# Performance work log

Measured on AMD Instinct MI355X. Metric: run time of the kernel, lower is better.

## Reference

```python
import jax, jax.numpy as jnp
import numpy as np

GAMMA = 0.99
EPS = 1e-05
B, D, K, C = 65536, 512, 1024, 100


def setup_inputs() -> dict:
    key = jax.random.key(0)
    k1, k2, k3, k4, k5 = jax.random.split(key, 5)
    return {
        "batch_vectors": jax.random.normal(k1, (B, D), dtype=jnp.float32),
        "batch_keys_id": jax.random.randint(k2, (B,), 0, C, dtype=jnp.int32),
        "weight": jax.random.normal(k3, (D, K), dtype=jnp.float32),
        "cluster_size": jnp.ones((K,), dtype=jnp.float32),
        "embed_avg": jax.random.normal(k4, (D, K), dtype=jnp.float32),
        "hist": jax.random.uniform(k5, (K, C), dtype=jnp.float32),
    }


def reference(batch_vectors, batch_keys_id, weight, cluster_size, embed_avg, hist):
    # --- find_nearest_centroids: euclidean distance to each codebook column ---
    x_sq = jnp.sum(batch_vectors * batch_vectors, axis=1, keepdims=True)      # [B,1]
    w_sq = jnp.sum(weight * weight, axis=0, keepdims=True)                    # [1,K]
    d2 = x_sq - 2.0 * (batch_vectors @ weight) + w_sq                         # [B,K]
    dist = jnp.sqrt(jnp.maximum(d2, 0.0))
    argmin = jnp.argmin(dist, axis=-1)                                        # [B]

    # --- one-hot counts and embed_sum (scatter-add form of flatten @ onehot) ---
    n_idx_choice = jax.ops.segment_sum(
        jnp.ones((B,), dtype=batch_vectors.dtype), argmin, num_segments=K)    # [K]
    n_idx_choice = jnp.where(n_idx_choice == 0, 1.0, n_idx_choice)
    embed_sum = jax.ops.segment_sum(batch_vectors, argmin, num_segments=K).T  # [D,K]

    # --- EMA updates ---
    new_cluster_size = cluster_size * GAMMA + (1.0 - GAMMA) * n_idx_choice
    new_embed_avg = embed_avg * GAMMA + (1.0 - GAMMA) * embed_sum
    n = jnp.sum(new_cluster_size)
    cs_norm = (new_cluster_size + EPS) / (n + K * EPS) * n                    # [K]
    new_weight = new_embed_avg / cs_norm[None, :]                             # [D,K]

    # --- update_hist: per-cluster class histogram (scatter-add) ---
    batch_hist = jnp.zeros((K, C), dtype=hist.dtype).at[argmin, batch_keys_id].add(1.0)
    new_hist = hist * GAMMA + (1.0 - GAMMA) * batch_hist

    return new_weight, new_cluster_size, new_embed_avg, new_hist, argmin
```

## Files before the change

### kernel.cpp

```cpp
#include <hip/hip_runtime.h>
#include <hip/hip_fp16.h>


#define NB 65536
#define ND 512
#define NK 1024
#define NC 100
#define TAU 0.25f
#define FLAG_CAP 16384
#define FROWS 8
#define GROWS 128

typedef unsigned int u32;
typedef unsigned short u16;
typedef unsigned long long u64;
typedef __attribute__((ext_vector_type(8))) _Float16 half8v;
typedef __attribute__((ext_vector_type(4))) float f32x4;

#define OFF_COUNTS   0
#define OFF_CURSOR   1024
#define OFF_BHIST    2048
#define OFF_FLAGCNT  104448
#define OFF_WSQ      104512
#define OFF_ZERO_END 105536
#define OFF_FLAGLIST 105536
#define OFF_FKEYS    121920
#define OFF_CSNORM   154688
#define OFF_OFFSETS  155712
#define OFF_ARGMIN   156736
#define OFF_ORDER    222272
#define OFF_KORDER   287808
#define OFF_WTHI     353344
#define OFF_WT32     615488
#define OFF_XH       1139776
#define OFF_ESUM     17916992

__device__ inline f32x4 mfma16f(half8v a, half8v b, f32x4 c) {
  return __builtin_amdgcn_mfma_f32_16x16x32_f16(a, b, c, 0, 0, 0);
}

__device__ __forceinline__ void gl_lds16(const u16* g, u16* l) {
  __builtin_amdgcn_global_load_lds(
      (const __attribute__((address_space(1))) u32*)g,
      (__attribute__((address_space(3))) u32*)l, 16, 0, 0);
}

__device__ inline u32 f32_sortable(float f) {
  u32 b = __float_as_uint(f);
  return (b & 0x80000000u) ? ~b : (b | 0x80000000u);
}

__device__ inline half8v cvt8_f16(const float4& a, const float4& b) {
  half8v h;
  h[0] = (_Float16)a.x; h[1] = (_Float16)a.y;
  h[2] = (_Float16)a.z; h[3] = (_Float16)a.w;
  h[4] = (_Float16)b.x; h[5] = (_Float16)b.y;
  h[6] = (_Float16)b.z; h[7] = (_Float16)b.w;
  return h;
}

__global__ __launch_bounds__(256) void prep_x(const float* __restrict__ X,
                                              u16* __restrict__ Xh) {
  size_t i = ((size_t)blockIdx.x * 256 + threadIdx.x) * 8;
  float4 a = *(const float4*)(X + i);
  float4 b = *(const float4*)(X + i + 4);
  *(half8v*)(Xh + i) = cvt8_f16(a, b);
}

__global__ __launch_bounds__(256) void prep_w(const float* __restrict__ W,
                                              u16* __restrict__ Wthi,
                                              float* __restrict__ Wt32,
                                              float* __restrict__ wsq) {
  __shared__ float tile[32][33];
  int db = blockIdx.x & 15;
  int kb = blockIdx.x >> 4;
  int tx = threadIdx.x & 31, ty = threadIdx.x >> 5;
  float s = 0.f;
#pragma unroll
  for (int i = 0; i < 4; ++i) {
    int d = db * 32 + ty + 8 * i;
    float wv = W[(size_t)d * NK + kb * 32 + tx];
    tile[ty + 8 * i][tx] = wv;
    s += wv * wv;
  }
  atomicAdd(&wsq[kb * 32 + tx], s);
  __syncthreads();
#pragma unroll
  for (int i = 0; i < 4; ++i) {
    int kl = ty + 8 * i;
    float f = tile[tx][kl];
    size_t o = (size_t)(kb * 32 + kl) * ND + db * 32 + tx;
    Wt32[o] = f;
    Wthi[o] = __half_as_ushort(__float2half(f));
  }
}

__global__ __launch_bounds__(256, 2) void argmin_pair(
    const u16* __restrict__ Xh, const u16* __restrict__ Wthi,
    const float* __restrict__ wsq, const int* __restrict__ cls,
    int* __restrict__ argmin_i, float* __restrict__ argmin_f,
    int* __restrict__ counts, float* __restrict__ bhist,
    int* __restrict__ flagCnt, int* __restrict__ flagList) {
  __shared__ __align__(16) u16 Ah[2 * 128 * 64];
  __shared__ __align__(16) u16 Bh[2 * 256 * 32];
  __shared__ float wsq_s[NK];
  __shared__ float redV[128][2];
  __shared__ float redS[128][2];
  __shared__ int redI[128][2];

  const int t = threadIdx.x;
  const int lane = t & 63;
  const int w = t >> 6;
  const int g = lane >> 4;
  const int l15 = lane & 15;
  const int wrb = (w >> 1) * 64;
  const int wcb = (w & 1) * 128;
  const int brow = blockIdx.x * 128;

#pragma unroll
  for (int i = 0; i < 4; ++i) wsq_s[t + 256 * i] = wsq[t + 256 * i];

  const int sub = lane >> 3;
  const int c8p = lane & 7;
  const size_t asrc = (size_t)(brow + w * 32 + sub) * ND + (size_t)((c8p ^ sub) * 8);

  const int rp = lane >> 2;
  const int bcl = (lane & 3) ^ (rp & 3);
  const size_t bsrc = (size_t)(w * 64 + rp) * ND + (size_t)(bcl * 8);

  int aofs[2];
#pragma unroll
  for (int kk = 0; kk < 2; ++kk)
    aofs[kk] = (wrb + l15) * 64 + (((kk * 4 + g) ^ (l15 & 7)) * 8);
  const int bofs = (wcb + l15) * 32 + ((g ^ (l15 & 3)) * 8);

  float bestV[4][4], secV[4][4];
  int bestI[4][4];
#pragma unroll
  for (int m = 0; m < 4; ++m)
#pragma unroll
    for (int r = 0; r < 4; ++r) {
      bestV[m][r] = 3.4e38f; secV[m][r] = 3.4e38f; bestI[m][r] = 0;
    }

  f32x4 acc[4][8];
#pragma unroll
  for (int m = 0; m < 4; ++m)
#pragma unroll
    for (int n = 0; n < 8; ++n) acc[m][n] = (f32x4)0.f;

#define ISSUE_A(kc_, ab_)                                                \
  {                                                                      \
    const u16* as_ = Xh + asrc + (kc_) * 64;                             \
    u16* ad_ = Ah + (ab_) * 8192 + w * 32 * 64;                          \
    _Pragma("unroll")                                                    \
    for (int q = 0; q < 4; ++q)                                          \
      gl_lds16(as_ + (size_t)(q * 8) * ND, ad_ + q * 8 * 64);            \
  }
#define ISSUE_B(ct_, sk_, bb_)                                           \
  {                                                                      \
    const u16* bs_ = Wthi + (size_t)(ct_) * 256 * ND + bsrc + (sk_) * 32;\
    u16* bd_ = Bh + (bb_) * 8192 + w * 64 * 32;                          \
    _Pragma("unroll")                                                    \
    for (int q = 0; q < 4; ++q)                                          \
      gl_lds16(bs_ + (size_t)(q * 16) * ND, bd_ + q * 16 * 32);          \
  }
#define DRAIN asm volatile("s_waitcnt vmcnt(0) lgkmcnt(0)" ::: "memory")

  ISSUE_A(0, 0);
  ISSUE_B(0, 0, 0);
  DRAIN;
  __syncthreads();

  for (int s = 0; s < 64; ++s) {
    const int sk = s & 15;
    const int kpar = s & 1;
    const int abuf = (s >> 1) & 1;
    const int bbuf = s & 1;
    if (s < 63) {
      const int s1 = s + 1;
      ISSUE_B(s1 >> 4, s1 & 15, s1 & 1);
      if (s & 1) ISSUE_A(((s1 & 15) >> 1), (s1 >> 1) & 1);
    }
    const u16* Ab = Ah + abuf * 8192;
    const u16* Bb = Bh + bbuf * 8192;
    {
      half8v a_h[4];
#pragma unroll
      for (int m = 0; m < 4; ++m)
        a_h[m] = *(const half8v*)&Ab[aofs[kpar] + m * 1024];
#pragma unroll
      for (int n = 0; n < 8; ++n) {
        half8v b_h = *(const half8v*)&Bb[bofs + n * 512];
#pragma unroll
        for (int m = 0; m < 4; ++m)
          acc[m][n] = mfma16f(a_h[m], b_h, acc[m][n]);
      }
    }
    if (sk == 15) {
      const int ct = s >> 4;
#pragma unroll
      for (int n = 0; n < 8; ++n) {
        int col = ct * 256 + wcb + 16 * n + l15;
        float wq = wsq_s[col];
#pragma unroll
        for (int m = 0; m < 4; ++m)
#pragma unroll
          for (int r = 0; r < 4; ++r) {
            float v = wq - 2.0f * acc[m][n][r];
            if (v < bestV[m][r]) {
              secV[m][r] = bestV[m][r];
              bestV[m][r] = v;
              bestI[m][r] = col;
            } else if (v < secV[m][r]) {
              secV[m][r] = v;
            }
          }
      }
#pragma unroll
      for (int m = 0; m < 4; ++m)
#pragma unroll
        for (int n = 0; n < 8; ++n) acc[m][n] = (f32x4)0.f;
    }
    DRAIN;
    __syncthreads();
  }
#undef ISSUE_A
#undef ISSUE_B
#undef DRAIN

#pragma unroll
  for (int m = 0; m < 4; ++m)
#pragma unroll
    for (int r = 0; r < 4; ++r) {
      float v = bestV[m][r];
      float sec = secV[m][r];
      int idx = bestI[m][r];
#pragma unroll
      for (int mask = 1; mask < 16; mask <<= 1) {
        float ov = __shfl_xor(v, mask, 64);
        float os = __shfl_xor(sec, mask, 64);
        int oi = __shfl_xor(idx, mask, 64);
        float nsec = fminf(fminf(sec, os), fmaxf(v, ov));
        if (ov < v || (ov == v && oi < idx)) { v = ov; idx = oi; }
        sec = nsec;
      }
      if (l15 == 0) {
        int rowl = wrb + 16 * m + 4 * g + r;
        redV[rowl][w & 1] = v;
        redS[rowl][w & 1] = sec;
        redI[rowl][w & 1] = idx;
      }
    }
  __syncthreads();
  if (t < 128) {
    float v0 = redV[t][0], v1 = redV[t][1];
    float s0 = redS[t][0], s1 = redS[t][1];
    int i0 = redI[t][0], i1 = redI[t][1];
    float bv, sec;
    int bi;
    if (v1 < v0 || (v1 == v0 && i1 < i0)) { bv = v1; bi = i1; }
    else { bv = v0; bi = i0; }
    sec = fminf(fminf(s0, s1), fmaxf(v0, v1));
    int b = brow + t;
    argmin_i[b] = bi;
    argmin_f[b] = (float)bi;
    atomicAdd(&counts[bi], 1);
    atomicAdd(&bhist[(size_t)bi * NC + cls[b]], 1.0f);
    if (sec - bv < TAU) {
      int slot = atomicAdd(flagCnt, 1);
      if (slot < FLAG_CAP) flagList[slot] = b;
    }
  }
}

__global__ __launch_bounds__(256) void fixup_score(
    const float* __restrict__ X, const float* __restrict__ Wt32,
    const float* __restrict__ wsq, const int* __restrict__ flagCnt,
    const int* __restrict__ flagList, u64* __restrict__ fkeys) {
  __shared__ float xs[FROWS][ND];
  __shared__ int rows[FROWS];
  __shared__ u64 wred[4][FROWS];
  int n = *flagCnt;
  if (n > FLAG_CAP) n = FLAG_CAP;
  int r0 = blockIdx.x * FROWS;
  if (r0 >= n) return;
  int nr = n - r0; if (nr > FROWS) nr = FROWS;
  int t = threadIdx.x;
  if (t < FROWS) rows[t] = flagList[r0 + (t < nr ? t : 0)];
  __syncthreads();
  for (int j = t; j < FROWS * (ND / 4); j += 256) {
    int r = j >> 7, c = j & 127;
    ((float4*)xs[r])[c] = ((const float4*)(X + (size_t)rows[r] * ND))[c];
  }
  __syncthreads();

  const int k0 = t * 4;
  const float4* w0 = (const float4*)(Wt32 + (size_t)(k0 + 0) * ND);
  const float4* w1 = (const float4*)(Wt32 + (size_t)(k0 + 1) * ND);
  const float4* w2 = (const float4*)(Wt32 + (size_t)(k0 + 2) * ND);
  const float4* w3 = (const float4*)(Wt32 + (size_t)(k0 + 3) * ND);
  float a[4][FROWS];
#pragma unroll
  for (int kk = 0; kk < 4; ++kk)
#pragma unroll
    for (int r = 0; r < FROWS; ++r) a[kk][r] = 0.f;

  for (int d = 0; d < ND / 4; ++d) {
    float4 v0 = w0[d], v1 = w1[d], v2 = w2[d], v3 = w3[d];
#pragma unroll
    for (int r = 0; r < FROWS; ++r) {
      float4 x4 = ((const float4*)xs[r])[d];
      a[0][r] += x4.x * v0.x + x4.y * v0.y + x4.z * v0.z + x4.w * v0.w;
      a[1][r] += x4.x * v1.x + x4.y * v1.y + x4.z * v1.z + x4.w * v1.w;
      a[2][r] += x4.x * v2.x + x4.y * v2.y + x4.z * v2.z + x4.w * v2.w;
      a[3][r] += x4.x * v3.x + x4.y * v3.y + x4.z * v3.z + x4.w * v3.w;
    }
  }

  float wq0 = wsq[k0], wq1 = wsq[k0 + 1], wq2 = wsq[k0 + 2], wq3 = wsq[k0 + 3];
  const int wv_ = t >> 6, lane = t & 63;
#pragma unroll
  for (int r = 0; r < FROWS; ++r) {
    float bv = wq0 - 2.0f * a[0][r];
    int bk = k0;
    float v;
    v = wq1 - 2.0f * a[1][r]; if (v < bv) { bv = v; bk = k0 + 1; }
    v = wq2 - 2.0f * a[2][r]; if (v < bv) { bv = v; bk = k0 + 2; }
    v = wq3 - 2.0f * a[3][r]; if (v < bv) { bv = v; bk = k0 + 3; }
    u64 key = ((u64)f32_sortable(bv) << 32) | (u32)bk;
#pragma unroll
    for (int m = 1; m < 64; m <<= 1) {
      u64 o = __shfl_xor(key, m, 64);
      if (o < key) key = o;
    }
    if (lane == 0) wred[wv_][r] = key;
  }
  __syncthreads();
  if (t < nr) {
    u64 k = wred[0][t];
    if (wred[1][t] < k) k = wred[1][t];
    if (wred[2][t] < k) k = wred[2][t];
    if (wred[3][t] < k) k = wred[3][t];
    fkeys[r0 + t] = k;
  }
}

__global__ __launch_bounds__(256) void fixup_apply(
    const int* __restrict__ flagCnt, const int* __restrict__ flagList,
    const u64* __restrict__ fkeys, const int* __restrict__ cls,
    int* __restrict__ argmin_i, float* __restrict__ argmin_f,
    int* __restrict__ counts, float* __restrict__ bhist) {
  int n = *flagCnt;
  if (n > FLAG_CAP) n = FLAG_CAP;
  int s = blockIdx.x * 256 + threadIdx.x;
  if (s >= n) return;
  int row = flagList[s];
  int nk = (int)(u32)(fkeys[s] & 0xffffffffu);
  int old = argmin_i[row];
  if (nk != old) {
    argmin_i[row] = nk;
    argmin_f[row] = (float)nk;
    atomicSub(&counts[old], 1);
    atomicAdd(&counts[nk], 1);
    int c = cls[row];
    atomicAdd(&bhist[(size_t)old * NC + c], -1.0f);
    atomicAdd(&bhist[(size_t)nk * NC + c], 1.0f);
  }
}

__global__ __launch_bounds__(1024) void scan_kernel(
    const int* __restrict__ counts, const float* __restrict__ cluster_size,
    float* __restrict__ out_ncs, float* __restrict__ csnorm,
    int* __restrict__ offsets) {
  __shared__ float wsum[16];
  __shared__ int wcnt[16];
  int t = threadIdx.x, lane = t & 63, wv = t >> 6;
  int cnt = counts[t];
  float ncs = cluster_size[t] * 0.99f + 0.01f * (cnt == 0 ? 1.0f : (float)cnt);
  out_ncs[t] = ncs;

  float s = ncs;
#pragma unroll
  for (int m = 1; m < 64; m <<= 1) s += __shfl_xor(s, m, 64);
  int ic = cnt;
#pragma unroll
  for (int o = 1; o < 64; o <<= 1) {
    int v = __shfl_up(ic, o, 64);
    if (lane >= o) ic += v;
  }
  if (lane == 63) { wsum[wv] = s; wcnt[wv] = ic; }
  __syncthreads();
  float n = 0.f;
  int coff = 0;
  for (int i = 0; i < 16; ++i) {
    n += wsum[i];
    if (i < wv) coff += wcnt[i];
  }
  csnorm[t] = (ncs + 1e-5f) / (n + 1024.0f * 1e-5f) * n;
  offsets[t] = coff + ic - cnt;
}

__global__ __launch_bounds__(256) void reorder_kernel(
    const int* __restrict__ argmin_i, const int* __restrict__ offsets,
    int* __restrict__ cursor, int* __restrict__ order,
    int* __restrict__ korder) {
  int b = blockIdx.x * 256 + threadIdx.x;
  int k = argmin_i[b];
  int pos = atomicAdd(&cursor[k], 1);
  int o = offsets[k] + pos;
  order[o] = b;
  korder[o] = k;
}

__global__ __launch_bounds__(256) void gather_runs(
    const float* __restrict__ X, const int* __restrict__ order,
    const int* __restrict__ korder, float* __restrict__ esum) {
  __shared__ int so[GROWS];
  __shared__ int sk[GROWS];
  int t = threadIdx.x;
  int base = blockIdx.x * GROWS;
  if (t < GROWS) {
    so[t] = order[base + t];
    sk[t] = korder[base + t];
  }
  __syncthreads();
  float a0 = 0.f, a1 = 0.f;
  int curk = sk[0];
#pragma unroll 8
  for (int m = 0; m < GROWS; ++m) {
    int k = sk[m];
    if (k != curk) {
      atomicAdd(&esum[(size_t)curk * ND + 2 * t], a0);
      atomicAdd(&esum[(size_t)curk * ND + 2 * t + 1], a1);
      a0 = 0.f; a1 = 0.f; curk = k;
    }
    float2 v = *(const float2*)(X + (size_t)so[m] * ND + 2 * t);
    a0 += v.x;
    a1 += v.y;
  }
  atomicAdd(&esum[(size_t)curk * ND + 2 * t], a0);
  atomicAdd(&esum[(size_t)curk * ND + 2 * t + 1], a1);
}

__global__ __launch_bounds__(256) void ema_embed_kernel(
    const float* __restrict__ esum, const float* __restrict__ embed_avg,
    const float* __restrict__ csnorm, float* __restrict__ out_w,
    float* __restrict__ out_ea) {
  __shared__ float tile[32][33];
  int kb = blockIdx.x & 31;
  int db = blockIdx.x >> 5;
  int tx = threadIdx.x & 31, ty = threadIdx.x >> 5;
#pragma unroll
  for (int i = 0; i < 4; ++i) {
    int kl = ty + i * 8;
    tile[kl][tx] = esum[(size_t)(kb * 32 + kl) * ND + db * 32 + tx];
  }
  __syncthreads();
#pragma unroll
  for (int i = 0; i < 4; ++i) {
    int d = db * 32 + ty + i * 8;
    int k = kb * 32 + tx;
    size_t idx = (size_t)d * NK + k;
    float nea = embed_avg[idx] * 0.99f + 0.01f * tile[tx][ty + i * 8];
    out_ea[idx] = nea;
    out_w[idx] = nea / csnorm[k];
  }
}

__global__ __launch_bounds__(256) void hist_kernel(const float* __restrict__ hist,
                                                   const float* __restrict__ bhist,
                                                   float* __restrict__ out_hist) {
  int i = blockIdx.x * 256 + threadIdx.x;
  out_hist[i] = hist[i] * 0.99f + 0.01f * bhist[i];
}

extern "C" void kernel_launch(void* const* d_in, const int* in_sizes, int n_in,
                              void* d_out, int out_size, void* d_ws, size_t ws_size,
                              hipStream_t stream) {
  const float* X = (const float*)d_in[0];
  const int* cls = (const int*)d_in[1];
  const float* W = (const float*)d_in[2];
  const float* cluster_size = (const float*)d_in[3];
  const float* embed_avg = (const float*)d_in[4];
  const float* hist = (const float*)d_in[5];

  float* wsf = (float*)d_ws;
  int* wsi = (int*)d_ws;
  int* counts = wsi + OFF_COUNTS;
  int* cursor = wsi + OFF_CURSOR;
  float* bhist = wsf + OFF_BHIST;
  int* flagCnt = wsi + OFF_FLAGCNT;
  float* wsq = wsf + OFF_WSQ;
  int* flagList = wsi + OFF_FLAGLIST;
  u64* fkeys = (u64*)(wsf + OFF_FKEYS);
  float* csnorm = wsf + OFF_CSNORM;
  int* offsets = wsi + OFF_OFFSETS;
  int* argmin_i = wsi + OFF_ARGMIN;
  int* order = wsi + OFF_ORDER;
  int* korder = wsi + OFF_KORDER;
  u16* Wthi = (u16*)(wsf + OFF_WTHI);
  float* Wt32 = wsf + OFF_WT32;
  u16* Xh = (u16*)(wsf + OFF_XH);
  float* esum = wsf + OFF_ESUM;

  float* out = (float*)d_out;
  float* out_w = out;
  float* out_ncs = out + (size_t)ND * NK;
  float* out_ea = out_ncs + NK;
  float* out_hist = out_ea + (size_t)ND * NK;
  float* out_arg = out_hist + (size_t)NK * NC;

  hipMemsetAsync(d_ws, 0, (size_t)OFF_ZERO_END * 4, stream);
  hipMemsetAsync(esum, 0, (size_t)NK * ND * 4, stream);

  prep_w<<<512, 256, 0, stream>>>(W, Wthi, Wt32, wsq);
  prep_x<<<NB * ND / 8 / 256, 256, 0, stream>>>(X, Xh);
  argmin_pair<<<NB / 128, 256, 0, stream>>>(Xh, Wthi, wsq, cls, argmin_i,
                                            out_arg, counts, bhist, flagCnt,
                                            flagList);
  fixup_score<<<FLAG_CAP / FROWS, 256, 0, stream>>>(X, Wt32, wsq, flagCnt,
                                                    flagList, fkeys);
  fixup_apply<<<FLAG_CAP / 256, 256, 0, stream>>>(flagCnt, flagList, fkeys, cls,
                                                  argmin_i, out_arg, counts,
                                                  bhist);
  scan_kernel<<<1, 1024, 0, stream>>>(counts, cluster_size, out_ncs, csnorm,
                                      offsets);
  reorder_kernel<<<NB / 256, 256, 0, stream>>>(argmin_i, offsets, cursor, order,
                                               korder);
  gather_runs<<<NB / GROWS, 256, 0, stream>>>(X, order, korder, esum);
  ema_embed_kernel<<<(NK / 32) * (ND / 32), 256, 0, stream>>>(
      esum, embed_avg, csnorm, out_w, out_ea);
  hist_kernel<<<(NK * NC) / 256, 256, 0, stream>>>(hist, bhist, out_hist);
}
```

Before: 369.2 us.

## Fuse prep, fixup and EMA/hist kernels; fold esum zeroing; relayout B tile in LDS

Merges prep_w and prep_x into one launch, fuses fixup_score with fixup_apply so the fkeys buffer goes away, and folds hist_kernel into the EMA kernel. It also drops the esum memset by zeroing esum inside reorder_kernel. The shared-memory layout of the W tile in argmin_pair changes from 256x32 to paired rows stored 128x64 with a new swizzle, which alters the LDS access pattern. Together these cut launch overhead and an extra memset, at the risk of layout or swizzle errors in the GEMM path.

```diff
diff --git a/kernel.cpp b/kernel.cpp
--- a/kernel.cpp
+++ b/kernel.cpp
@@ -59,22 +59,24 @@
   return h;
 }
 
-__global__ __launch_bounds__(256) void prep_x(const float* __restrict__ X,
-                                              u16* __restrict__ Xh) {
-  size_t i = ((size_t)blockIdx.x * 256 + threadIdx.x) * 8;
-  float4 a = *(const float4*)(X + i);
-  float4 b = *(const float4*)(X + i + 4);
-  *(half8v*)(Xh + i) = cvt8_f16(a, b);
-}
-
-__global__ __launch_bounds__(256) void prep_w(const float* __restrict__ W,
-                                              u16* __restrict__ Wthi,
-                                              float* __restrict__ Wt32,
-                                              float* __restrict__ wsq) {
+__global__ __launch_bounds__(256) void prep_all(const float* __restrict__ W,
+                                                const float* __restrict__ X,
+                                                u16* __restrict__ Wthi,
+                                                float* __restrict__ Wt32,
+                                                u16* __restrict__ Xh,
+                                                float* __restrict__ wsq) {
   __shared__ float tile[32][33];
+  int t = threadIdx.x;
+  if (blockIdx.x >= 512) {
+    size_t i = ((size_t)(blockIdx.x - 512) * 256 + t) * 8;
+    float4 a = *(const float4*)(X + i);
+    float4 b = *(const float4*)(X + i + 4);
+    *(half8v*)(Xh + i) = cvt8_f16(a, b);
+    return;
+  }
   int db = blockIdx.x & 15;
   int kb = blockIdx.x >> 4;
-  int tx = threadIdx.x & 31, ty = threadIdx.x >> 5;
+  int tx = t & 31, ty = t >> 5;
   float s = 0.f;
 #pragma unroll
   for (int i = 0; i < 4; ++i) {
@@ -102,7 +104,7 @@
     int* __restrict__ counts, float* __restrict__ bhist,
     int* __restrict__ flagCnt, int* __restrict__ flagList) {
   __shared__ __align__(16) u16 Ah[2 * 128 * 64];
-  __shared__ __align__(16) u16 Bh[2 * 256 * 32];
+  __shared__ __align__(16) u16 Bh[2 * 128 * 64];
   __shared__ float wsq_s[NK];
   __shared__ float redV[128][2];
   __shared__ float redS[128][2];
@@ -124,15 +126,15 @@
   const int c8p = lane & 7;
   const size_t asrc = (size_t)(brow + w * 32 + sub) * ND + (size_t)((c8p ^ sub) * 8);
 
-  const int rp = lane >> 2;
-  const int bcl = (lane & 3) ^ (rp & 3);
-  const size_t bsrc = (size_t)(w * 64 + rp) * ND + (size_t)(bcl * 8);
+  const size_t bsrc = (size_t)(2 * (w * 32 + sub) + (c8p >> 2)) * ND +
+                      (size_t)(((c8p & 3) ^ (sub & 3)) * 8);
 
   int aofs[2];
 #pragma unroll
   for (int kk = 0; kk < 2; ++kk)
     aofs[kk] = (wrb + l15) * 64 + (((kk * 4 + g) ^ (l15 & 7)) * 8);
-  const int bofs = (wcb + l15) * 32 + ((g ^ (l15 & 3)) * 8);
+  const int bofs = wcb * 32 + (l15 >> 1) * 64 + (l15 & 1) * 32 +
+                   ((g ^ ((l15 >> 1) & 3)) * 8);
 
   float bestV[4][4], secV[4][4];
   int bestI[4][4];
@@ -160,10 +162,10 @@
 #define ISSUE_B(ct_, sk_, bb_)                                           \
   {                                                                      \
     const u16* bs_ = Wthi + (size_t)(ct_) * 256 * ND + bsrc + (sk_) * 32;\
-    u16* bd_ = Bh + (bb_) * 8192 + w * 64 * 32;                          \
+    u16* bd_ = Bh + (bb_) * 8192 + w * 32 * 64;                          \
     _Pragma("unroll")                                                    \
     for (int q = 0; q < 4; ++q)                                          \
-      gl_lds16(bs_ + (size_t)(q * 16) * ND, bd_ + q * 16 * 32);          \
+      gl_lds16(bs_ + (size_t)(q * 16) * ND, bd_ + q * 8 * 64);           \
   }
 #define DRAIN asm volatile("s_waitcnt vmcnt(0) lgkmcnt(0)" ::: "memory")
 
@@ -274,10 +276,12 @@
   }
 }
 
-__global__ __launch_bounds__(256) void fixup_score(
+__global__ __launch_bounds__(256) void fixup_kernel(
     const float* __restrict__ X, const float* __restrict__ Wt32,
     const float* __restrict__ wsq, const int* __restrict__ flagCnt,
-    const int* __restrict__ flagList, u64* __restrict__ fkeys) {
+    const int* __restrict__ flagList, const int* __restrict__ cls,
+    int* __restrict__ argmin_i, float* __restrict__ argmin_f,
+    int* __restrict__ counts, float* __restrict__ bhist) {
   __shared__ float xs[FROWS][ND];
   __shared__ int rows[FROWS];
   __shared__ u64 wred[4][FROWS];
@@ -342,30 +346,18 @@
     if (wred[1][t] < k) k = wred[1][t];
     if (wred[2][t] < k) k = wred[2][t];
     if (wred[3][t] < k) k = wred[3][t];
-    fkeys[r0 + t] = k;
-  }
-}
-
-__global__ __launch_bounds__(256) void fixup_apply(
-    const int* __restrict__ flagCnt, const int* __restrict__ flagList,
-    const u64* __restrict__ fkeys, const int* __restrict__ cls,
-    int* __restrict__ argmin_i, float* __restrict__ argmin_f,
-    int* __restrict__ counts, float* __restrict__ bhist) {
-  int n = *flagCnt;
-  if (n > FLAG_CAP) n = FLAG_CAP;
-  int s = blockIdx.x * 256 + threadIdx.x;
-  if (s >= n) return;
-  int row = flagList[s];
-  int nk = (int)(u32)(fkeys[s] & 0xffffffffu);
-  int old = argmin_i[row];
-  if (nk != old) {
-    argmin_i[row] = nk;
-    argmin_f[row] = (float)nk;
-    atomicSub(&counts[old], 1);
-    atomicAdd(&counts[nk], 1);
-    int c = cls[row];
-    atomicAdd(&bhist[(size_t)old * NC + c], -1.0f);
-    atomicAdd(&bhist[(size_t)nk * NC + c], 1.0f);
+    int nk = (int)(u32)(k & 0xffffffffu);
+    int row = rows[t];
+    int old = argmin_i[row];
+    if (nk != old) {
+      argmin_i[row] = nk;
+      argmin_f[row] = (float)nk;
+      atomicSub(&counts[old], 1);
+      atomicAdd(&counts[nk], 1);
+      int c = cls[row];
+      atomicAdd(&bhist[(size_t)old * NC + c], -1.0f);
+      atomicAdd(&bhist[(size_t)nk * NC + c], 1.0f);
+    }
   }
 }
 
@@ -404,8 +396,11 @@
 __global__ __launch_bounds__(256) void reorder_kernel(
     const int* __restrict__ argmin_i, const int* __restrict__ offsets,
     int* __restrict__ cursor, int* __restrict__ order,
-    int* __restrict__ korder) {
+    int* __restrict__ korder, float* __restrict__ esum) {
   int b = blockIdx.x * 256 + threadIdx.x;
+  float4 z = make_float4(0.f, 0.f, 0.f, 0.f);
+  *(float4*)(esum + (size_t)b * 8) = z;
+  *(float4*)(esum + (size_t)b * 8 + 4) = z;
   int k = argmin_i[b];
   int pos = atomicAdd(&cursor[k], 1);
   int o = offsets[k] + pos;
@@ -443,14 +438,21 @@
   atomicAdd(&esum[(size_t)curk * ND + 2 * t + 1], a1);
 }
 
-__global__ __launch_bounds__(256) void ema_embed_kernel(
+__global__ __launch_bounds__(256) void ema_hist_kernel(
     const float* __restrict__ esum, const float* __restrict__ embed_avg,
-    const float* __restrict__ csnorm, float* __restrict__ out_w,
-    float* __restrict__ out_ea) {
+    const float* __restrict__ csnorm, const float* __restrict__ hist,
+    const float* __restrict__ bhist, float* __restrict__ out_w,
+    float* __restrict__ out_ea, float* __restrict__ out_hist) {
   __shared__ float tile[32][33];
+  int t = threadIdx.x;
+  if (blockIdx.x >= 512) {
+    int i = (blockIdx.x - 512) * 256 + t;
+    out_hist[i] = hist[i] * 0.99f + 0.01f * bhist[i];
+    return;
+  }
   int kb = blockIdx.x & 31;
   int db = blockIdx.x >> 5;
-  int tx = threadIdx.x & 31, ty = threadIdx.x >> 5;
+  int tx = t & 31, ty = t >> 5;
 #pragma unroll
   for (int i = 0; i < 4; ++i) {
     int kl = ty + i * 8;
@@ -466,13 +468,6 @@
     out_ea[idx] = nea;
     out_w[idx] = nea / csnorm[k];
   }
-}
-
-__global__ __launch_bounds__(256) void hist_kernel(const float* __restrict__ hist,
-                                                   const float* __restrict__ bhist,
-                                                   float* __restrict__ out_hist) {
-  int i = blockIdx.x * 256 + threadIdx.x;
-  out_hist[i] = hist[i] * 0.99f + 0.01f * bhist[i];
 }
 
 extern "C" void kernel_launch(void* const* d_in, const int* in_sizes, int n_in,
@@ -493,7 +488,6 @@
   int* flagCnt = wsi + OFF_FLAGCNT;
   float* wsq = wsf + OFF_WSQ;
   int* flagList = wsi + OFF_FLAGLIST;
-  u64* fkeys = (u64*)(wsf + OFF_FKEYS);
   float* csnorm = wsf + OFF_CSNORM;
   int* offsets = wsi + OFF_OFFSETS;
   int* argmin_i = wsi + OFF_ARGMIN;
@@ -512,24 +506,20 @@
   float* out_arg = out_hist + (size_t)NK * NC;
 
   hipMemsetAsync(d_ws, 0, (size_t)OFF_ZERO_END * 4, stream);
-  hipMemsetAsync(esum, 0, (size_t)NK * ND * 4, stream);
-
-  prep_w<<<512, 256, 0, stream>>>(W, Wthi, Wt32, wsq);
-  prep_x<<<NB * ND / 8 / 256, 256, 0, stream>>>(X, Xh);
+
+  prep_all<<<512 + NB * ND / 8 / 256, 256, 0, stream>>>(W, X, Wthi, Wt32, Xh,
+                                                        wsq);
   argmin_pair<<<NB / 128, 256, 0, stream>>>(Xh, Wthi, wsq, cls, argmin_i,
                                             out_arg, counts, bhist, flagCnt,
                                             flagList);
-  fixup_score<<<FLAG_CAP / FROWS, 256, 0, stream>>>(X, Wt32, wsq, flagCnt,
-                                                    flagList, fkeys);
-  fixup_apply<<<FLAG_CAP / 256, 256, 0, stream>>>(flagCnt, flagList, fkeys, cls,
-                                                  argmin_i, out_arg, counts,
-                                                  bhist);
+  fixup_kernel<<<FLAG_CAP / FROWS, 256, 0, stream>>>(X, Wt32, wsq, flagCnt,
+                                                     flagList, cls, argmin_i,
+                                                     out_arg, counts, bhist);
   scan_kernel<<<1, 1024, 0, stream>>>(counts, cluster_size, out_ncs, csnorm,
                                       offsets);
   reorder_kernel<<<NB / 256, 256, 0, stream>>>(argmin_i, offsets, cursor, order,
-                                               korder);
+                                               korder, esum);
   gather_runs<<<NB / GROWS, 256, 0, stream>>>(X, order, korder, esum);
-  ema_embed_kernel<<<(NK / 32) * (ND / 32), 256, 0, stream>>>(
-      esum, embed_avg, csnorm, out_w, out_ea);
-  hist_kernel<<<(NK * NC) / 256, 256, 0, stream>>>(hist, bhist, out_hist);
-}
+  ema_hist_kernel<<<512 + (NK * NC) / 256, 256, 0, stream>>>(
+      esum, embed_avg, csnorm, hist, bhist, out_w, out_ea, out_hist);
+}
```

Result: faster. 360.9 us (-2.3%).
